# Kernel optimization log

Hardware: AMD Instinct MI355X
Metric: run time of the kernel (lower is better)

## Reference

```python
import jax, jax.numpy as jnp
import numpy as np

SIGMA = 0.03   # self.sig = [0.03] in the original module
EPS = 1e-12    # guard for degenerate (zero-area) faces from random indices


def _mesh_quantities(V, F):
    """Face centers, areas (|0.5*cross|) and unit normals. V:[Nv,3], F:[Nf,3] int."""
    v0 = V[F[:, 0]]
    v1 = V[F[:, 1]]
    v2 = V[F[:, 2]]
    C = (v0 + v1 + v2) / 3.0                      # [Nf,3] face centers
    N = 0.5 * jnp.cross(v1 - v0, v2 - v0)         # [Nf,3] area-weighted normals
    L = jnp.linalg.norm(N, axis=-1)               # [Nf]  face areas
    Nn = N / jnp.maximum(L, EPS)[:, None]         # [Nf,3] unit normals
    return C, L, Nn


def _kernel_sum(Cx, Lx, Nx, Cy, Ly, Ny, gamma):
    """sum_ij Lx_i Ly_j exp(-gamma |Cx_i-Cy_j|^2) <Nx_i,Ny_j>^2  (unoriented Gauss-squared varifold kernel)."""
    d2 = (jnp.sum(Cx * Cx, -1)[:, None]
          + jnp.sum(Cy * Cy, -1)[None, :]
          - 2.0 * Cx @ Cy.T)                       # [F,F]
    dot = Nx @ Ny.T                                # [F,F]
    K = jnp.exp(-gamma * d2) * (dot * dot)
    return jnp.einsum('i,ij,j->', Lx, K, Ly)


def reference(predictions, targets, faces):
    gamma = 1.0 / (SIGMA * SIGMA)

    def per_sample(carry, xy):
        Vs, Vt = xy
        Cs, Ls, Ns = _mesh_quantities(Vs, faces)
        Ct, Lt, Nt = _mesh_quantities(Vt, faces)
        li = (_kernel_sum(Cs, Ls, Ns, Cs, Ls, Ns, gamma)
              + _kernel_sum(Ct, Lt, Nt, Ct, Lt, Nt, gamma)
              - 2.0 * _kernel_sum(Cs, Ls, Ns, Ct, Lt, Nt, gamma))
        return carry + li, None

    total, _ = jax.lax.scan(per_sample,
                            jnp.asarray(0.0, predictions.dtype),
                            (predictions, targets))
    return (total / predictions.shape[0])[None]   # shape [1], like torch.Tensor([0.0])


def setup_inputs() -> dict:
    key = jax.random.key(0)
    k1, k2, k3 = jax.random.split(key, 3)
    B, NV, NF = 4, 5023, 9976
    # scale 0.02 so inter-face distances are commensurate with sigma=0.03
    predictions = 0.02 * jax.random.normal(k1, (B, NV, 3), dtype=jnp.float32)
    targets = 0.02 * jax.random.normal(k2, (B, NV, 3), dtype=jnp.float32)
    faces = jax.random.randint(k3, (NF, 3), 0, NV, dtype=jnp.int32)
    return {"predictions": predictions, "targets": targets, "faces": faces}
```

## Files before the change

### kernel.cpp

```cpp
#include <hip/hip_runtime.h>


#define NVERT 5023
#define NFACE 9976
#define BATCH 4
#define HALFP 9984
#define NTP   (2 * HALFP)
#define NTOT  (BATCH * NTP)
#define NCH   624
#define NPAN  156
#define SPLITS 13

constexpr float GAMMA = 1.0f / (0.03f * 0.03f);
constexpr float LOG2E = 1.4426950408889634f;
constexpr float EPSV  = 1e-12f;

typedef _Float16 half8_t  __attribute__((ext_vector_type(8)));
typedef float    f32x16   __attribute__((ext_vector_type(16)));

__global__ __launch_bounds__(256)
void face_quant_kernel(const float* __restrict__ pred,
                       const float* __restrict__ targ,
                       const int*   __restrict__ faces,
                       _Float16*    __restrict__ fd,
                       float*       __restrict__ out) {
    int idx = blockIdx.x * 256 + threadIdx.x;
    if (idx == 0) out[0] = 0.0f;
    if (idx >= NTOT) return;

    int b     = idx / NTP;
    int s     = idx - b * NTP;
    int which = (s >= HALFP) ? 1 : 0;
    int f     = s - which * HALFP;

    _Float16* arec = fd + (size_t)idx * 32;
    _Float16* brec = fd + (size_t)NTOT * 32 + (size_t)idx * 32;

    if (f >= NFACE) {
        half8_t z = {};
        *(half8_t*)(arec + 0) = z; *(half8_t*)(arec + 8)  = z;
        *(half8_t*)(arec + 16) = z; *(half8_t*)(arec + 24) = z;
        *(half8_t*)(brec + 0) = z; *(half8_t*)(brec + 8)  = z;
        *(half8_t*)(brec + 16) = z; *(half8_t*)(brec + 24) = z;
        return;
    }

    const float* V = (which ? targ : pred) + (size_t)b * NVERT * 3;
    int i0 = faces[f * 3 + 0];
    int i1 = faces[f * 3 + 1];
    int i2 = faces[f * 3 + 2];

    float v0x = V[i0*3+0], v0y = V[i0*3+1], v0z = V[i0*3+2];
    float v1x = V[i1*3+0], v1y = V[i1*3+1], v1z = V[i1*3+2];
    float v2x = V[i2*3+0], v2y = V[i2*3+1], v2z = V[i2*3+2];

    const float third = 1.0f / 3.0f;
    float cx = (v0x + v1x + v2x) * third;
    float cy = (v0y + v1y + v2y) * third;
    float cz = (v0z + v1z + v2z) * third;

    float e1x = v1x - v0x, e1y = v1y - v0y, e1z = v1z - v0z;
    float e2x = v2x - v0x, e2y = v2y - v0y, e2z = v2z - v0z;

    float nx = 0.5f * (e1y * e2z - e1z * e2y);
    float ny = 0.5f * (e1z * e2x - e1x * e2z);
    float nz = 0.5f * (e1x * e2y - e1y * e2x);

    float L   = sqrtf(nx*nx + ny*ny + nz*nz);
    float inv = 1.0f / fmaxf(L, EPSV);
    float sc  = inv * sqrtf(L);
    float mx = nx * sc, my = ny * sc, mz = nz * sc;

    const float TG = 2.0f * GAMMA * LOG2E;
    float tgx = TG * cx, tgy = TG * cy, tgz = TG * cz;
    float cq  = -GAMMA * LOG2E * (cx*cx + cy*cy + cz*cz);

    _Float16 TGxh = (_Float16)tgx; _Float16 TGxl = (_Float16)(tgx - (float)TGxh);
    _Float16 TGyh = (_Float16)tgy; _Float16 TGyl = (_Float16)(tgy - (float)TGyh);
    _Float16 TGzh = (_Float16)tgz; _Float16 TGzl = (_Float16)(tgz - (float)TGzh);
    _Float16 Cxh  = (_Float16)cx;  _Float16 Cxl  = (_Float16)(cx  - (float)Cxh);
    _Float16 Cyh  = (_Float16)cy;  _Float16 Cyl  = (_Float16)(cy  - (float)Cyh);
    _Float16 Czh  = (_Float16)cz;  _Float16 Czl  = (_Float16)(cz  - (float)Czh);
    _Float16 cqh  = (_Float16)cq;  _Float16 cql  = (_Float16)(cq  - (float)cqh);
    _Float16 mxh  = (_Float16)mx;  _Float16 mxl  = (_Float16)(mx  - (float)mxh);
    _Float16 myh  = (_Float16)my;  _Float16 myl  = (_Float16)(my  - (float)myh);
    _Float16 mzh  = (_Float16)mz;  _Float16 mzl  = (_Float16)(mz  - (float)mzh);
    _Float16 one  = (_Float16)1.0f;
    _Float16 zz   = (_Float16)0.0f;

    half8_t ta0 = {TGxh, TGyh, TGzh, TGxl, TGyl, TGzl, TGxh, TGyh};
    half8_t ta1 = {TGzh, TGxl, TGyl, TGzl, cqh,  cql,  one,  one };
    half8_t da0 = {mxh,  myh,  mzh,  mxl,  myl,  mzl,  mxh,  myh };
    half8_t da1 = {mzh,  mxl,  myl,  mzl,  zz,   zz,   zz,   zz  };
    half8_t tb0 = {Cxh,  Cyh,  Czh,  Cxh,  Cyh,  Czh,  Cxl,  Cyl };
    half8_t tb1 = {Czl,  Cxl,  Cyl,  Czl,  one,  one,  cqh,  cql };
    half8_t db0 = {mxh,  myh,  mzh,  mxh,  myh,  mzh,  mxl,  myl };
    half8_t db1 = {mzl,  mxl,  myl,  mzl,  zz,   zz,   zz,   zz  };

    *(half8_t*)(arec + 0)  = ta0;  *(half8_t*)(arec + 8)  = ta1;
    *(half8_t*)(arec + 16) = da0;  *(half8_t*)(arec + 24) = da1;
    *(half8_t*)(brec + 0)  = tb0;  *(half8_t*)(brec + 8)  = tb1;
    *(half8_t*)(brec + 16) = db0;  *(half8_t*)(brec + 24) = db1;
}

__device__ __forceinline__ half8_t ld8(const _Float16* p) {
    return *(const half8_t*)p;
}

__global__ __launch_bounds__(256, 6)
void pair_sum_kernel(const _Float16* __restrict__ fd,
                     float*          __restrict__ out) {
    const int b       = blockIdx.z;
    const int pairIdx = blockIdx.x / SPLITS;
    const int s       = blockIdx.x % SPLITS;

    const _Float16* Arec = fd;
    const _Float16* Brec = fd + (size_t)NTOT * 32;

    const int lane = threadIdx.x & 63;
    const int w    = threadIdx.x >> 6;
    const int col  = lane & 31;
    const int koff = (lane >> 5) * 8;

    const size_t bface = (size_t)b * NTP;
    const size_t JSTEP = (size_t)SPLITS * 32 * 32;

    float acc = 0.0f;

    #pragma unroll 1
    for (int h = 0; h < 2; ++h) {
        const int   P  = h ? (NPAN - 1 - pairIdx) : pairIdx;
        const int   c0 = 4 * P;
        const float si = (P < NPAN / 2) ? 1.0f : -1.0f;
        const int   iters = (NCH - c0 - s + SPLITS - 1) / SPLITS;
        if (iters <= 0) continue;

        const _Float16* ap = Arec + (bface + (size_t)(P * 128 + w * 32 + col)) * 32 + koff;
        half8_t aT = ld8(ap);
        half8_t aD = ld8(ap + 16);

        const _Float16* pB = Brec + (bface + (size_t)((c0 + s) * 32 + col)) * 32 + koff;
        half8_t bT = ld8(pB);
        half8_t bD = ld8(pB + 16);

        #pragma unroll 1
        for (int k = 0; k < iters; ++k) {
            const _Float16* pN = (k + 1 < iters) ? (pB + JSTEP) : pB;
            half8_t nT = ld8(pN);
            half8_t nD = ld8(pN + 16);
            pB = pN;

            f32x16 z = {};
            f32x16 T = __builtin_amdgcn_mfma_f32_32x32x16_f16(aT, bT, z, 0, 0, 0);
            f32x16 D = __builtin_amdgcn_mfma_f32_32x32x16_f16(aD, bD, z, 0, 0, 0);

            float ts0 = 0.f, ts1 = 0.f;
            #pragma unroll
            for (int r = 0; r < 16; r += 2) {
                float e0 = __builtin_amdgcn_exp2f(T[r]);
                float d0 = D[r];
                ts0 = fmaf(e0, d0 * d0, ts0);
                float e1 = __builtin_amdgcn_exp2f(T[r + 1]);
                float d1 = D[r + 1];
                ts1 = fmaf(e1, d1 * d1, ts1);
            }

            const int   jc  = c0 + s + SPLITS * k;
            const float sj  = (jc < NCH / 2) ? si : -si;
            const float wgt = (k == 0 && s < 4) ? 1.0f : 2.0f;
            acc = fmaf(sj * wgt * (1.0f / BATCH), ts0 + ts1, acc);

            bT = nT; bD = nD;
        }
    }

    #pragma unroll
    for (int off = 32; off > 0; off >>= 1)
        acc += __shfl_down(acc, off, 64);

    __shared__ float wsum[4];
    if (lane == 0) wsum[w] = acc;
    __syncthreads();
    if (threadIdx.x == 0)
        atomicAdd(out, wsum[0] + wsum[1] + wsum[2] + wsum[3]);
}

extern "C" void kernel_launch(void* const* d_in, const int* in_sizes, int n_in,
                              void* d_out, int out_size, void* d_ws, size_t ws_size,
                              hipStream_t stream) {
    const float* pred  = (const float*)d_in[0];
    const float* targ  = (const float*)d_in[1];
    const int*   faces = (const int*)d_in[2];
    float*       out   = (float*)d_out;
    _Float16*    fd    = (_Float16*)d_ws;

    face_quant_kernel<<<(NTOT + 255) / 256, 256, 0, stream>>>(
        pred, targ, faces, fd, out);

    dim3 grid((NPAN / 2) * SPLITS, 1, BATCH);
    pair_sum_kernel<<<grid, 256, 0, stream>>>(fd, out);
}
```

Measured before the change: 174.3 us.

## Software-pipeline MFMA with exp epilogue using double-buffered tiles and packed math

Restructures the inner loop so the MFMA for the next tile is issued before the exp/square epilogue of the previous tile. This overlaps matrix-core latency with VALU transcendental work. The epilogue now uses two-wide float vectors so the compiler can emit packed multiply/FMA, and the 1/BATCH scaling moves out of the loop. Occupancy hint drops from 6 to 4 blocks per CU to leave room for the extra live accumulator registers, which may reduce latency hiding across waves.

Result: faster. 168.8 us (-3.2%).

```diff
diff --git a/kernel.cpp b/kernel.cpp
--- a/kernel.cpp
+++ b/kernel.cpp
@@ -17,6 +17,7 @@
 
 typedef _Float16 half8_t  __attribute__((ext_vector_type(8)));
 typedef float    f32x16   __attribute__((ext_vector_type(16)));
+typedef float    f32x2    __attribute__((ext_vector_type(2)));
 
 __global__ __launch_bounds__(256)
 void face_quant_kernel(const float* __restrict__ pred,
@@ -107,7 +108,7 @@
     return *(const half8_t*)p;
 }
 
-__global__ __launch_bounds__(256, 6)
+__global__ __launch_bounds__(256, 4)
 void pair_sum_kernel(const _Float16* __restrict__ fd,
                      float*          __restrict__ out) {
     const int b       = blockIdx.z;
@@ -139,40 +140,70 @@
         half8_t aT = ld8(ap);
         half8_t aD = ld8(ap + 16);
 
+        #define FAC(k_) (si * (((c0 + s + SPLITS * (k_)) < NCH / 2) ? 1.0f : -1.0f) \
+                            * (((k_) == 0 && s < 4) ? 1.0f : 2.0f))
+
+        #define EPILOGUE(T_, D_, k_)                                           \
+        {                                                                      \
+            f32x2 ts2 = {0.f, 0.f};                                            \
+            _Pragma("unroll")                                                  \
+            for (int r = 0; r < 16; r += 2) {                                  \
+                f32x2 ee = {__builtin_amdgcn_exp2f((T_)[r]),                   \
+                            __builtin_amdgcn_exp2f((T_)[r + 1])};              \
+                f32x2 dd = {(D_)[r], (D_)[r + 1]};                             \
+                dd = dd * dd;                                                  \
+                ts2 = ee * dd + ts2;                                           \
+            }                                                                  \
+            acc = fmaf(FAC(k_), ts2.x + ts2.y, acc);                           \
+        }
+
         const _Float16* pB = Brec + (bface + (size_t)((c0 + s) * 32 + col)) * 32 + koff;
-        half8_t bT = ld8(pB);
-        half8_t bD = ld8(pB + 16);
-
+        half8_t bT0 = ld8(pB);
+        half8_t bD0 = ld8(pB + 16);
+
+        f32x16 z  = {};
+        f32x16 T0 = __builtin_amdgcn_mfma_f32_32x32x16_f16(aT, bT0, z, 0, 0, 0);
+        f32x16 D0 = __builtin_amdgcn_mfma_f32_32x32x16_f16(aD, bD0, z, 0, 0, 0);
+
+        const _Float16* pB1 = (iters > 1) ? (pB + JSTEP) : pB;
+        half8_t bT1 = ld8(pB1);
+        half8_t bD1 = ld8(pB1 + 16);
+        pB = pB1;
+
+        int k = 0;
         #pragma unroll 1
-        for (int k = 0; k < iters; ++k) {
-            const _Float16* pN = (k + 1 < iters) ? (pB + JSTEP) : pB;
-            half8_t nT = ld8(pN);
-            half8_t nD = ld8(pN + 16);
+        for (; k + 2 < iters; k += 2) {
+            f32x16 T1 = __builtin_amdgcn_mfma_f32_32x32x16_f16(aT, bT1, z, 0, 0, 0);
+            f32x16 D1 = __builtin_amdgcn_mfma_f32_32x32x16_f16(aD, bD1, z, 0, 0, 0);
+            pB += JSTEP;
+            bT0 = ld8(pB);
+            bD0 = ld8(pB + 16);
+
+            EPILOGUE(T0, D0, k);
+
+            T0 = __builtin_amdgcn_mfma_f32_32x32x16_f16(aT, bT0, z, 0, 0, 0);
+            D0 = __builtin_amdgcn_mfma_f32_32x32x16_f16(aD, bD0, z, 0, 0, 0);
+            const _Float16* pN = (k + 3 < iters) ? (pB + JSTEP) : pB;
+            bT1 = ld8(pN);
+            bD1 = ld8(pN + 16);
             pB = pN;
 
-            f32x16 z = {};
-            f32x16 T = __builtin_amdgcn_mfma_f32_32x32x16_f16(aT, bT, z, 0, 0, 0);
-            f32x16 D = __builtin_amdgcn_mfma_f32_32x32x16_f16(aD, bD, z, 0, 0, 0);
-
-            float ts0 = 0.f, ts1 = 0.f;
-            #pragma unroll
-            for (int r = 0; r < 16; r += 2) {
-                float e0 = __builtin_amdgcn_exp2f(T[r]);
-                float d0 = D[r];
-                ts0 = fmaf(e0, d0 * d0, ts0);
-                float e1 = __builtin_amdgcn_exp2f(T[r + 1]);
-                float d1 = D[r + 1];
-                ts1 = fmaf(e1, d1 * d1, ts1);
-            }
-
-            const int   jc  = c0 + s + SPLITS * k;
-            const float sj  = (jc < NCH / 2) ? si : -si;
-            const float wgt = (k == 0 && s < 4) ? 1.0f : 2.0f;
-            acc = fmaf(sj * wgt * (1.0f / BATCH), ts0 + ts1, acc);
-
-            bT = nT; bD = nD;
+            EPILOGUE(T1, D1, k + 1);
         }
+
+        if (iters - k == 2) {
+            f32x16 T1 = __builtin_amdgcn_mfma_f32_32x32x16_f16(aT, bT1, z, 0, 0, 0);
+            f32x16 D1 = __builtin_amdgcn_mfma_f32_32x32x16_f16(aD, bD1, z, 0, 0, 0);
+            EPILOGUE(T0, D0, k);
+            EPILOGUE(T1, D1, k + 1);
+        } else {
+            EPILOGUE(T0, D0, k);
+        }
+        #undef EPILOGUE
+        #undef FAC
     }
+
+    acc *= (1.0f / BATCH);
 
     #pragma unroll
     for (int off = 32; off > 0; off >>= 1)
```

## Double the row panel per wave to reuse B tiles across two MFMA tiles

Applied to the files above, without the earlier changes.

Each wave now holds two 32-row A tiles: panels grow to 256 faces and splits to 26. Every loaded B tile feeds four MFMAs instead of two, which halves B traffic per unit of work. The exp/square accumulation uses packed two-wide float vectors so the compiler can emit packed multiplies and FMAs. The zero accumulator and the batch scaling are hoisted out of the loop. The cost is more registers per thread, so the occupancy hint drops from 6 to 4 waves, and the grid is coarser.

Result: faster. 157.2 us, median of 2 (-9.8%).

```diff
diff --git a/kernel.cpp b/kernel.cpp
--- a/kernel.cpp
+++ b/kernel.cpp
@@ -8,8 +8,8 @@
 #define NTP   (2 * HALFP)
 #define NTOT  (BATCH * NTP)
 #define NCH   624
-#define NPAN  156
-#define SPLITS 13
+#define NPAN  78
+#define SPLITS 26
 
 constexpr float GAMMA = 1.0f / (0.03f * 0.03f);
 constexpr float LOG2E = 1.4426950408889634f;
@@ -17,6 +17,7 @@
 
 typedef _Float16 half8_t  __attribute__((ext_vector_type(8)));
 typedef float    f32x16   __attribute__((ext_vector_type(16)));
+typedef float    f32x2    __attribute__((ext_vector_type(2)));
 
 __global__ __launch_bounds__(256)
 void face_quant_kernel(const float* __restrict__ pred,
@@ -107,7 +108,7 @@
     return *(const half8_t*)p;
 }
 
-__global__ __launch_bounds__(256, 6)
+__global__ __launch_bounds__(256, 4)
 void pair_sum_kernel(const _Float16* __restrict__ fd,
                      float*          __restrict__ out) {
     const int b       = blockIdx.z;
@@ -130,18 +131,23 @@
     #pragma unroll 1
     for (int h = 0; h < 2; ++h) {
         const int   P  = h ? (NPAN - 1 - pairIdx) : pairIdx;
-        const int   c0 = 4 * P;
+        const int   c0 = 8 * P;
         const float si = (P < NPAN / 2) ? 1.0f : -1.0f;
         const int   iters = (NCH - c0 - s + SPLITS - 1) / SPLITS;
         if (iters <= 0) continue;
 
-        const _Float16* ap = Arec + (bface + (size_t)(P * 128 + w * 32 + col)) * 32 + koff;
-        half8_t aT = ld8(ap);
-        half8_t aD = ld8(ap + 16);
+        const _Float16* ap0 = Arec + (bface + (size_t)(P * 256 + w * 32 + col)) * 32 + koff;
+        const _Float16* ap1 = ap0 + (size_t)128 * 32;
+        half8_t aT0 = ld8(ap0);
+        half8_t aD0 = ld8(ap0 + 16);
+        half8_t aT1 = ld8(ap1);
+        half8_t aD1 = ld8(ap1 + 16);
 
         const _Float16* pB = Brec + (bface + (size_t)((c0 + s) * 32 + col)) * 32 + koff;
         half8_t bT = ld8(pB);
         half8_t bD = ld8(pB + 16);
+
+        f32x16 z = {};
 
         #pragma unroll 1
         for (int k = 0; k < iters; ++k) {
@@ -150,29 +156,36 @@
             half8_t nD = ld8(pN + 16);
             pB = pN;
 
-            f32x16 z = {};
-            f32x16 T = __builtin_amdgcn_mfma_f32_32x32x16_f16(aT, bT, z, 0, 0, 0);
-            f32x16 D = __builtin_amdgcn_mfma_f32_32x32x16_f16(aD, bD, z, 0, 0, 0);
-
-            float ts0 = 0.f, ts1 = 0.f;
+            f32x16 T0 = __builtin_amdgcn_mfma_f32_32x32x16_f16(aT0, bT, z, 0, 0, 0);
+            f32x16 D0 = __builtin_amdgcn_mfma_f32_32x32x16_f16(aD0, bD, z, 0, 0, 0);
+            f32x16 T1 = __builtin_amdgcn_mfma_f32_32x32x16_f16(aT1, bT, z, 0, 0, 0);
+            f32x16 D1 = __builtin_amdgcn_mfma_f32_32x32x16_f16(aD1, bD, z, 0, 0, 0);
+
+            f32x2 ts0 = {0.f, 0.f}, ts1 = {0.f, 0.f};
             #pragma unroll
             for (int r = 0; r < 16; r += 2) {
-                float e0 = __builtin_amdgcn_exp2f(T[r]);
-                float d0 = D[r];
-                ts0 = fmaf(e0, d0 * d0, ts0);
-                float e1 = __builtin_amdgcn_exp2f(T[r + 1]);
-                float d1 = D[r + 1];
-                ts1 = fmaf(e1, d1 * d1, ts1);
+                f32x2 e0 = {__builtin_amdgcn_exp2f(T0[r]),
+                            __builtin_amdgcn_exp2f(T0[r + 1])};
+                f32x2 d0 = {D0[r], D0[r + 1]};
+                d0 = d0 * d0;
+                ts0 = e0 * d0 + ts0;
+                f32x2 e1 = {__builtin_amdgcn_exp2f(T1[r]),
+                            __builtin_amdgcn_exp2f(T1[r + 1])};
+                f32x2 d1 = {D1[r], D1[r + 1]};
+                d1 = d1 * d1;
+                ts1 = e1 * d1 + ts1;
             }
 
             const int   jc  = c0 + s + SPLITS * k;
             const float sj  = (jc < NCH / 2) ? si : -si;
-            const float wgt = (k == 0 && s < 4) ? 1.0f : 2.0f;
-            acc = fmaf(sj * wgt * (1.0f / BATCH), ts0 + ts1, acc);
+            const float wgt = (k == 0 && s < 8) ? 1.0f : 2.0f;
+            acc = fmaf(sj * wgt, ts0.x + ts0.y + ts1.x + ts1.y, acc);
 
             bT = nT; bD = nD;
         }
     }
+
+    acc *= (1.0f / BATCH);
 
     #pragma unroll
     for (int off = 32; off > 0; off >>= 1)
```
